# Optimization experiments

Hardware: AMD Instinct MI355X
Metric: run time of the kernel (lower is better)

## Reference

```python
import jax, jax.numpy as jnp
import numpy as np

T, B, D, H, HH, OUT = 512, 128, 256, 1024, 256, 128
EPS = 1e-3

def _ln(x, gamma, beta):
    # layer_norm over feature dim, eps=0.001, matching torch reciprocal(sqrt(var+eps))
    m = jnp.mean(x, -1, keepdims=True)
    xs = x - m
    v = jnp.mean(xs * xs, -1, keepdims=True)
    return gamma * xs * jax.lax.rsqrt(v + EPS) + beta

def _ln_all(h, base, units, gamma, beta):
    # normalize each of `base` gate blocks independently over `units`
    b = h.shape[0]
    hr = h.reshape(b, base, units)
    m = jnp.mean(hr, -1, keepdims=True)
    xs = hr - m
    v = jnp.mean(xs * xs, -1, keepdims=True)
    hn = (xs * jax.lax.rsqrt(v + EPS)).reshape(b, base * units)
    return gamma * hn + beta

def setup_inputs() -> dict:
    key = jax.random.key(0)
    ks = jax.random.split(key, 12)
    return {
        "x": jax.random.normal(ks[0], (T, B, D), jnp.float32),
        "Wx": jax.random.normal(ks[1], (4 * H, D), jnp.float32) * (1.0 / np.sqrt(D)),
        "Wh": jax.random.normal(ks[2], (4 * H, H), jnp.float32) * (1.0 / np.sqrt(H)),
        "bias": jax.random.normal(ks[3], (4 * H,), jnp.float32) * 0.1,
        "lna_gamma": jnp.ones((4 * H,), jnp.float32),
        "lna_beta": jnp.zeros((4 * H,), jnp.float32),
        "ln_gamma": jnp.ones((H,), jnp.float32),
        "ln_beta": jnp.zeros((H,), jnp.float32),
        "zb": jax.random.normal(ks[4], (4, HH, HH), jnp.float32) * 0.01,   # ib/jb/fb/ob _zb
        "zbeta": jax.random.normal(ks[5], (4, HH, H), jnp.float32) * 0.01, # ib/jb/fb/ob _beta
        "zw_w": jax.random.normal(ks[6], (8, HH, HH), jnp.float32) * 0.01, # ix,jx,fx,ox,ih,jh,fh,oh _zw_w
        "zw_b": jnp.ones((8, HH), jnp.float32),
        "alpha": jnp.full((8, HH, H), 0.1 / HH, jnp.float32) + jax.random.normal(ks[7], (8, HH, H), jnp.float32) * 1e-4,
        "hyp_Wx": jax.random.normal(ks[8], (4 * HH, D + H), jnp.float32) * (1.0 / np.sqrt(D + H)),
        "hyp_bx": jnp.zeros((4 * HH,), jnp.float32),
        "hyp_Wh": jax.random.normal(ks[9], (4 * HH, HH), jnp.float32) * (1.0 / np.sqrt(HH)),
        "hyp_bh": jnp.zeros((4 * HH,), jnp.float32),
        "hyp_lna_gamma": jnp.ones((4 * HH,), jnp.float32),
        "hyp_lna_beta": jnp.zeros((4 * HH,), jnp.float32),
        "hyp_ln_gamma": jnp.ones((HH,), jnp.float32),
        "hyp_ln_beta": jnp.zeros((HH,), jnp.float32),
        "fc_W": jax.random.normal(ks[10], (OUT, H), jnp.float32) * (1.0 / np.sqrt(H)),
        "fc_b": jnp.zeros((OUT,), jnp.float32),
    }

def reference(x, Wx, Wh, bias, lna_gamma, lna_beta, ln_gamma, ln_beta, zb, zbeta,
              zw_w, zw_b, alpha, hyp_Wx, hyp_bx, hyp_Wh, hyp_bh,
              hyp_lna_gamma, hyp_lna_beta, hyp_ln_gamma, hyp_ln_beta, fc_W, fc_b):
    b4 = bias.reshape(4, H)

    def step(carry, xt):
        h, c, hh, ch = carry  # main (B,H), hyper (B,HH)
        # ---- hypernetwork LSTM cell (layer-norm LSTM) ----
        g = jnp.concatenate([xt, h], 1) @ hyp_Wx.T + hyp_bx + hh @ hyp_Wh.T + hyp_bh
        g = _ln_all(g, 4, HH, hyp_lna_gamma, hyp_lna_beta)
        hi, hf, hg, ho = jnp.split(g, 4, 1)  # ingate, forgetgate, cellgate, outgate
        ch_n = jax.nn.sigmoid(hf) * ch + jax.nn.sigmoid(hi) * jnp.tanh(hg)
        hyp = jax.nn.sigmoid(ho) * jnp.tanh(_ln(ch_n, hyp_ln_gamma, hyp_ln_beta))
        # ---- hyper-modulation: per-gate scale vectors and bias adjustments ----
        z = jnp.einsum('bq,kqp->kbp', hyp, zw_w) + zw_b[:, None, :]   # (8,B,HH)
        sc = jnp.einsum('kbp,kph->kbh', z, alpha)                     # (8,B,H)
        bz = jnp.einsum('bq,kqp->kbp', hyp, zb)                       # (4,B,HH)
        badj = jnp.einsum('kbp,kph->kbh', bz, zbeta)                  # (4,B,H)
        # ---- main LSTM gates (order i, j, f, o) ----
        xg = (xt @ Wx.T).reshape(B, 4, H).transpose(1, 0, 2)          # (4,B,H)
        hg2 = (h @ Wh.T).reshape(B, 4, H).transpose(1, 0, 2)          # (4,B,H)
        gates = sc[:4] * xg + sc[4:] * hg2 + b4[:, None, :] + badj    # (4,B,H)
        gates = _ln_all(gates.transpose(1, 0, 2).reshape(B, 4 * H), 4, H, lna_gamma, lna_beta)
        i, j, f, o = jnp.split(gates, 4, 1)
        c_n = jax.nn.sigmoid(f) * c + jax.nn.sigmoid(i) * jnp.tanh(j)
        h_n = jax.nn.sigmoid(o) * jnp.tanh(_ln(c_n, ln_gamma, ln_beta))
        return (h_n, c_n, hyp, ch_n), None

    init = (jnp.zeros((B, H), x.dtype), jnp.zeros((B, H), x.dtype),
            jnp.zeros((B, HH), x.dtype), jnp.zeros((B, HH), x.dtype))
    (h_f, _, _, _), _ = jax.lax.scan(step, init, x)
    return h_f @ fc_W.T + fc_b  # (B, OUT)
```

## Files before the change

### kernel.cpp

```cpp
#include <hip/hip_runtime.h>
#include <hip/hip_cooperative_groups.h>
#include <math.h>

namespace cg = cooperative_groups;

#define T_STEPS 512
#define BATCH   128
#define DIN     256
#define HMAIN   1024
#define HHYP    256
#define OUTN    128
#define EPS     1e-3f

#define KSPLIT_NONE (1<<30)

typedef __attribute__((ext_vector_type(4))) float f32x4;
typedef __attribute__((ext_vector_type(8))) short s16x8;

__device__ __forceinline__ float sigm(float x){ return 1.f/(1.f + expf(-x)); }

__device__ __forceinline__ unsigned short f2bf(float f){
    union { float f; unsigned u; } x; x.f = f;
    unsigned r = x.u + 0x7FFFu + ((x.u >> 16) & 1u);
    return (unsigned short)(r >> 16);
}

#define BM 32
#define BN 64
#define KT 32
__device__ void gemm_dev(const float* __restrict__ A1, int lda1, int ksplit,
                         const float* __restrict__ A2, int lda2,
                         const float* __restrict__ Bp, int ldb, int b_nk,
                         const float* __restrict__ bias,
                         float* __restrict__ C, int ldc,
                         int K, int k0, int mtile, int ntile)
{
    __shared__ __align__(16) float As[KT][BM+4];
    __shared__ __align__(16) float Bs[KT][BN+4];
    const int tid = threadIdx.x;
    const int mt = tid >> 4, nt = tid & 15;
    const int m0g = mtile*BM, n0g = ntile*BN;
    float acc[4][4];
    #pragma unroll
    for (int i=0;i<4;++i) { acc[i][0]=0;acc[i][1]=0;acc[i][2]=0;acc[i][3]=0; }
    for (int kt = 0; kt < K; kt += KT) {
        __syncthreads();
        #pragma unroll
        for (int i=0;i<8;++i){
            int e = tid + i*128;
            int m = e >> 5, k = e & 31;
            int gk = k0 + kt + k, gm = m0g + m;
            float v = (gk < ksplit) ? A1[(size_t)gm*lda1 + gk]
                                    : A2[(size_t)gm*lda2 + (gk - ksplit)];
            As[k][m] = v;
        }
        if (b_nk) {
            #pragma unroll
            for (int i=0;i<16;++i){
                int e = tid + i*128;
                int n = e >> 5, k = e & 31;
                Bs[k][n] = Bp[(size_t)(n0g + n)*ldb + (k0 + kt + k)];
            }
        } else {
            #pragma unroll
            for (int i=0;i<16;++i){
                int e = tid + i*128;
                int k = e >> 6, n = e & 63;
                Bs[k][n] = Bp[(size_t)(k0 + kt + k)*ldb + (n0g + n)];
            }
        }
        __syncthreads();
        #pragma unroll
        for (int k=0;k<KT;++k){
            float4 av = *(const float4*)(&As[k][4*mt]);
            float4 bv = *(const float4*)(&Bs[k][4*nt]);
            acc[0][0]+=av.x*bv.x; acc[0][1]+=av.x*bv.y; acc[0][2]+=av.x*bv.z; acc[0][3]+=av.x*bv.w;
            acc[1][0]+=av.y*bv.x; acc[1][1]+=av.y*bv.y; acc[1][2]+=av.y*bv.z; acc[1][3]+=av.y*bv.w;
            acc[2][0]+=av.z*bv.x; acc[2][1]+=av.z*bv.y; acc[2][2]+=av.z*bv.z; acc[2][3]+=av.z*bv.w;
            acc[3][0]+=av.w*bv.x; acc[3][1]+=av.w*bv.y; acc[3][2]+=av.w*bv.z; acc[3][3]+=av.w*bv.w;
        }
    }
    #pragma unroll
    for (int i=0;i<4;++i){
        int gm = m0g + 4*mt + i;
        #pragma unroll
        for (int j=0;j<4;++j){
            int gn = n0g + 4*nt + j;
            float v = acc[i][j];
            if (bias) v += bias[gn];
            C[(size_t)gm*ldc + gn] = v;
        }
    }
}

#define ASTR 40
__device__ void gemm_mfma(const float* __restrict__ A1, int lda1, int ksplit,
                          const float* __restrict__ A2, int lda2,
                          const unsigned short* __restrict__ B, int ldb,
                          const float* __restrict__ bias,
                          float* __restrict__ C, int ldc,
                          int K, int k0, int mtile, int ntile)
{
    __shared__ __align__(16) unsigned short As[32*ASTR];
    __shared__ __align__(16) unsigned short Bs[128*ASTR];
    const int tid = threadIdx.x;
    const int lane = tid & 63, w = tid >> 6;
    const int wm = (w >> 1) * 16, wn = (w & 1) * 64;
    const int fr = lane & 15, koff = (lane >> 4) * 8;
    const int m0g = mtile*32, n0g = ntile*128;

    f32x4 acc[4];
    #pragma unroll
    for (int j=0;j<4;++j) acc[j] = (f32x4){0.f,0.f,0.f,0.f};

    const int arow = tid >> 3, akc = (tid & 7) * 4;
    for (int kt = 0; kt < K; kt += 32) {
        __syncthreads();
        {
            int gk = k0 + kt + akc;
            int gm = m0g + arow;
            const float* src = (gk < ksplit) ? (A1 + (size_t)gm*lda1 + gk)
                                             : (A2 + (size_t)gm*lda2 + (gk - ksplit));
            float4 v = *(const float4*)src;
            unsigned short* d = &As[arow*ASTR + akc];
            d[0] = f2bf(v.x); d[1] = f2bf(v.y); d[2] = f2bf(v.z); d[3] = f2bf(v.w);
        }
        #pragma unroll
        for (int i=0;i<4;++i){
            int e = tid + i*256;
            int n = e >> 3, kc = (e & 7) * 4;
            ushort4 bv = *(const ushort4*)(B + (size_t)(n0g + n)*ldb + (k0 + kt + kc));
            unsigned short* d = &Bs[n*ASTR + kc];
            d[0] = bv.x; d[1] = bv.y; d[2] = bv.z; d[3] = bv.w;
        }
        __syncthreads();
        s16x8 af = *(const s16x8*)&As[(wm + fr)*ASTR + koff];
        #pragma unroll
        for (int j=0;j<4;++j){
            s16x8 bf = *(const s16x8*)&Bs[(wn + j*16 + fr)*ASTR + koff];
            acc[j] = __builtin_amdgcn_mfma_f32_16x16x32_bf16(af, bf, acc[j], 0, 0, 0);
        }
    }
    #pragma unroll
    for (int j=0;j<4;++j){
        int gn = n0g + wn + j*16 + fr;
        float bb = bias ? bias[gn] : 0.f;
        #pragma unroll
        for (int r=0;r<4;++r){
            int gm = m0g + wm + (lane >> 4)*4 + r;
            C[(size_t)gm*ldc + gn] = acc[j][r] + bb;
        }
    }
}

__global__ __launch_bounds__(256) void k_prep_convert(
    const float* __restrict__ hyp_Wx, const float* __restrict__ hyp_Wh,
    const float* __restrict__ hyp_bx, const float* __restrict__ hyp_bh,
    const float* __restrict__ Wx, const float* __restrict__ Wh,
    unsigned short* __restrict__ wcat1bf, unsigned short* __restrict__ wxbf,
    unsigned short* __restrict__ whbf, float* __restrict__ bias1,
    float* __restrict__ act1, float* __restrict__ c, float* __restrict__ ch)
{
    size_t i = (size_t)blockIdx.x*256 + threadIdx.x;
    if (i < 1572864u) {
        int n = (int)(i / 1536), k = (int)(i % 1536);
        float v = (k < 1280) ? hyp_Wx[(size_t)n*1280 + k] : hyp_Wh[(size_t)n*256 + (k-1280)];
        wcat1bf[i] = f2bf(v); return;
    }
    i -= 1572864u;
    if (i < 1048576u) { wxbf[i] = f2bf(Wx[i]); return; }
    i -= 1048576u;
    if (i < 4194304u) { whbf[i] = f2bf(Wh[i]); return; }
    i -= 4194304u;
    if (i < 1024u) { bias1[i] = hyp_bx[i] + hyp_bh[i]; return; }
    i -= 1024u;
    if (i < 163840u) { act1[i] = 0.f; return; }
    i -= 163840u;
    if (i < 131072u) { c[i] = 0.f; return; }
    i -= 131072u;
    if (i < 32768u) { ch[i] = 0.f; return; }
}

__global__ __launch_bounds__(128) void k_prep_wcomb(
    const float* __restrict__ zw_w, const float* __restrict__ zb,
    const float* __restrict__ alpha, const float* __restrict__ zbeta,
    float* __restrict__ wcombf32)
{
    int kk = blockIdx.z;
    const float* A = (kk < 8) ? (zw_w + (size_t)kk*65536) : (zb + (size_t)(kk-8)*65536);
    const float* Bm = (kk < 8) ? (alpha + (size_t)kk*262144) : (zbeta + (size_t)(kk-8)*262144);
    gemm_dev(A, 256, KSPLIT_NONE, A, 256, Bm, 1024, 0, nullptr,
             wcombf32 + (size_t)kk*262144, 1024, 256, 0, blockIdx.x, blockIdx.y);
}

__global__ __launch_bounds__(256) void k_prep_cvtcomb(
    const float* __restrict__ wcombf32, unsigned short* __restrict__ wcombbf)
{
    size_t i = (size_t)blockIdx.x*256 + threadIdx.x;
    if (i >= 3145728u) return;
    int kk = (int)(i / 262144u);
    int r  = (int)(i % 262144u);
    int n = r / 256, k = r % 256;
    wcombbf[i] = f2bf(wcombf32[(size_t)kk*262144 + (size_t)k*1024 + n]);
}

__global__ __launch_bounds__(256) void k_prep_bcomb(
    const float* __restrict__ zw_b, const float* __restrict__ alpha,
    float* __restrict__ bcomb)
{
    int k = blockIdx.x;
    int n = blockIdx.y*256 + threadIdx.x;
    float s = 0.f;
    for (int p=0;p<256;++p)
        s += zw_b[k*256+p] * alpha[(size_t)k*262144 + (size_t)p*1024 + n];
    bcomb[(size_t)k*1024 + n] = s;
}

__device__ __forceinline__ void breduce2(float& a, float& b, volatile float* buf, int tid){
    #pragma unroll
    for (int off = 32; off > 0; off >>= 1) { a += __shfl_xor(a, off); b += __shfl_xor(b, off); }
    __syncthreads();
    if ((tid & 63) == 0) { buf[(tid>>6)*2] = a; buf[(tid>>6)*2+1] = b; }
    __syncthreads();
    a = buf[0] + buf[2] + buf[4] + buf[6];
    b = buf[1] + buf[3] + buf[5] + buf[7];
}

__device__ __forceinline__ void hyper_cell_body(
    const float* __restrict__ lna_g, const float* __restrict__ lna_b,
    const float* __restrict__ ln_g, const float* __restrict__ ln_b,
    const float* __restrict__ gpart, const float* __restrict__ bias1,
    float* __restrict__ ch, float* __restrict__ act1, int b, int tid)
{
    __shared__ float buf[8];
    float v[4];
    #pragma unroll
    for (int g=0; g<4; ++g){
        int idx = b*1024 + g*256 + tid;
        v[g] = gpart[idx] + gpart[131072 + idx] + gpart[262144 + idx] + gpart[393216 + idx]
             + bias1[g*256 + tid];
    }
    #pragma unroll
    for (int g=0; g<4; ++g){
        float s = v[g], ss = v[g]*v[g];
        breduce2(s, ss, buf, tid);
        float m = s * (1.f/256.f);
        float var = ss * (1.f/256.f) - m*m;
        v[g] = (v[g]-m)*rsqrtf(var + EPS)*lna_g[g*256+tid] + lna_b[g*256+tid];
    }
    float chp = ch[b*256 + tid];
    float cn = sigm(v[1])*chp + sigm(v[0])*tanhf(v[2]);
    float s = cn, ss = cn*cn;
    breduce2(s, ss, buf, tid);
    float m = s*(1.f/256.f);
    float var = ss*(1.f/256.f) - m*m;
    float hn = sigm(v[3]) * tanhf((cn-m)*rsqrtf(var + EPS)*ln_g[tid] + ln_b[tid]);
    ch[b*256 + tid] = cn;
    act1[b*1280 + 1024 + tid] = hn;
}

__device__ __forceinline__ void main_cell_body(
    const float* __restrict__ bias4,
    const float* __restrict__ lna_g, const float* __restrict__ lna_b,
    const float* __restrict__ ln_g, const float* __restrict__ ln_b,
    const float* __restrict__ xghg, const float* __restrict__ scb,
    float* __restrict__ c, float* __restrict__ act1, int b, int tid)
{
    __shared__ float buf[8];
    float gn[4][4];
    #pragma unroll
    for (int k=0;k<4;++k){
        float pre[4]; float s=0.f, ss=0.f;
        #pragma unroll
        for (int j=0;j<4;++j){
            int h = j*256 + tid;
            int n = k*1024 + h;
            int bh = b*1024 + h;
            float xgv = xghg[b*4096 + n];
            float hgv = xghg[524288 + b*4096 + n];
            float p = scb[k*131072 + bh]*xgv + scb[(4+k)*131072 + bh]*hgv
                    + bias4[n] + scb[(8+k)*131072 + bh];
            pre[j] = p; s += p; ss += p*p;
        }
        breduce2(s, ss, buf, tid);
        float m = s*(1.f/1024.f);
        float var = ss*(1.f/1024.f) - m*m;
        float rs = rsqrtf(var + EPS);
        #pragma unroll
        for (int j=0;j<4;++j){
            int h=j*256+tid, n=k*1024+h;
            gn[k][j] = (pre[j]-m)*rs*lna_g[n] + lna_b[n];
        }
    }
    float cnv[4]; float s=0.f, ss=0.f;
    #pragma unroll
    for (int j=0;j<4;++j){
        int h=j*256+tid;
        float cv = c[b*1024+h];
        float x = sigm(gn[2][j])*cv + sigm(gn[0][j])*tanhf(gn[1][j]);
        cnv[j]=x; s+=x; ss+=x*x;
    }
    breduce2(s, ss, buf, tid);
    float m=s*(1.f/1024.f);
    float var=ss*(1.f/1024.f)-m*m;
    float rs=rsqrtf(var + EPS);
    #pragma unroll
    for (int j=0;j<4;++j){
        int h=j*256+tid;
        float hv = sigm(gn[3][j])*tanhf((cnv[j]-m)*rs*ln_g[h] + ln_b[h]);
        c[b*1024+h] = cnv[j];
        act1[b*1280 + h] = hv;
    }
}

__global__ __launch_bounds__(256) void k_step1(
    const float* __restrict__ xt, const float* __restrict__ act1,
    const unsigned short* __restrict__ wcat1bf,
    const unsigned short* __restrict__ wxbf, const unsigned short* __restrict__ whbf,
    float* __restrict__ gpart, float* __restrict__ xghg)
{
    int bid = blockIdx.x;
    if (bid < 128) {
        int sp = bid >> 5, r = bid & 31;
        gemm_mfma(xt, 256, 256, act1, 1280, wcat1bf, 1536, nullptr,
                  gpart + (size_t)sp*131072, 1024, 384, sp*384, r >> 3, r & 7);
    } else if (bid < 256) {
        int r = bid - 128;
        gemm_mfma(xt, 256, KSPLIT_NONE, xt, 256, wxbf, 256, nullptr,
                  xghg, 4096, 256, 0, r >> 5, r & 31);
    } else {
        int r = bid - 256;
        gemm_mfma(act1, 1280, KSPLIT_NONE, act1, 1280, whbf, 1024, nullptr,
                  xghg + 524288, 4096, 1024, 0, r >> 5, r & 31);
    }
}

__global__ __launch_bounds__(256) void k_step2(
    const float* __restrict__ act1, const unsigned short* __restrict__ wcombbf,
    const float* __restrict__ bcomb, float* __restrict__ scb)
{
    int bid = blockIdx.x;
    int kk = bid >> 5, r = bid & 31;
    const float* bias = (kk < 8) ? (bcomb + (size_t)kk*1024) : nullptr;
    gemm_mfma(act1 + 1024, 1280, KSPLIT_NONE, act1 + 1024, 1280,
              wcombbf + (size_t)kk*262144, 256, bias,
              scb + (size_t)kk*131072, 1024, 256, 0, r >> 3, r & 7);
}

__global__ __launch_bounds__(256) void k_hyper_cell(
    const float* __restrict__ lna_g, const float* __restrict__ lna_b,
    const float* __restrict__ ln_g, const float* __restrict__ ln_b,
    const float* __restrict__ gpart, const float* __restrict__ bias1,
    float* __restrict__ ch, float* __restrict__ act1)
{
    hyper_cell_body(lna_g, lna_b, ln_g, ln_b, gpart, bias1, ch, act1,
                    blockIdx.x, threadIdx.x);
}

__global__ __launch_bounds__(256) void k_main_cell(
    const float* __restrict__ bias4,
    const float* __restrict__ lna_g, const float* __restrict__ lna_b,
    const float* __restrict__ ln_g, const float* __restrict__ ln_b,
    const float* __restrict__ xghg, const float* __restrict__ scb,
    float* __restrict__ c, float* __restrict__ act1)
{
    main_cell_body(bias4, lna_g, lna_b, ln_g, ln_b, xghg, scb, c, act1,
                   blockIdx.x, threadIdx.x);
}

__global__ __launch_bounds__(256, 2) void k_persistent(
    const float* __restrict__ x,
    const unsigned short* __restrict__ wcat1bf,
    const unsigned short* __restrict__ wxbf,
    const unsigned short* __restrict__ whbf,
    const unsigned short* __restrict__ wcombbf,
    const float* __restrict__ bcomb,
    const float* __restrict__ bias1,
    const float* __restrict__ bias4,
    const float* __restrict__ lna_g, const float* __restrict__ lna_b,
    const float* __restrict__ ln_g, const float* __restrict__ ln_b,
    const float* __restrict__ hlna_g, const float* __restrict__ hlna_b,
    const float* __restrict__ hln_g, const float* __restrict__ hln_b,
    float* __restrict__ gpart, float* __restrict__ scb,
    float* __restrict__ xghg, float* __restrict__ act1,
    float* __restrict__ c, float* __restrict__ ch)
{
    cg::grid_group grid = cg::this_grid();
    const int bid = blockIdx.x;
    const int tid = threadIdx.x;

    for (int t = 0; t < T_STEPS; ++t) {
        const float* xt = x + (size_t)t*BATCH*DIN;

        if (bid < 128) {
            int sp = bid >> 5, r = bid & 31;
            gemm_mfma(xt, 256, 256, act1, 1280, wcat1bf, 1536, nullptr,
                      gpart + (size_t)sp*131072, 1024, 384, sp*384, r >> 3, r & 7);
        } else if (bid < 256) {
            int r = bid - 128;
            gemm_mfma(xt, 256, KSPLIT_NONE, xt, 256, wxbf, 256, nullptr,
                      xghg, 4096, 256, 0, r >> 5, r & 31);
        } else {
            int r = bid - 256;
            gemm_mfma(act1, 1280, KSPLIT_NONE, act1, 1280, whbf, 1024, nullptr,
                      xghg + 524288, 4096, 1024, 0, r >> 5, r & 31);
        }
        grid.sync();

        if (bid < 128)
            hyper_cell_body(hlna_g, hlna_b, hln_g, hln_b, gpart, bias1, ch, act1, bid, tid);
        grid.sync();

        {
            int kk = bid >> 5, r = bid & 31;
            const float* bias = (kk < 8) ? (bcomb + (size_t)kk*1024) : nullptr;
            gemm_mfma(act1 + 1024, 1280, KSPLIT_NONE, act1 + 1024, 1280,
                      wcombbf + (size_t)kk*262144, 256, bias,
                      scb + (size_t)kk*131072, 1024, 256, 0, r >> 3, r & 7);
        }
        grid.sync();

        if (bid < 128)
            main_cell_body(bias4, lna_g, lna_b, ln_g, ln_b, xghg, scb, c, act1, bid, tid);
        grid.sync();
    }
}

__global__ __launch_bounds__(128) void k_fc(
    const float* __restrict__ fcW, const float* __restrict__ fcb,
    const float* __restrict__ act1, float* __restrict__ out)
{
    int b = blockIdx.x, o = threadIdx.x;
    const float* h = act1 + (size_t)b*1280;
    float s = fcb[o];
    for (int k=0;k<1024;++k) s += h[k]*fcW[(size_t)o*1024 + k];
    out[b*OUTN + o] = s;
}

extern "C" void kernel_launch(void* const* d_in, const int* in_sizes, int n_in,
                              void* d_out, int out_size, void* d_ws, size_t ws_size,
                              hipStream_t stream)
{
    const float* x        = (const float*)d_in[0];
    const float* Wx       = (const float*)d_in[1];
    const float* Wh       = (const float*)d_in[2];
    const float* bias     = (const float*)d_in[3];
    const float* lna_g    = (const float*)d_in[4];
    const float* lna_b    = (const float*)d_in[5];
    const float* ln_g     = (const float*)d_in[6];
    const float* ln_b     = (const float*)d_in[7];
    const float* zb       = (const float*)d_in[8];
    const float* zbeta    = (const float*)d_in[9];
    const float* zw_w     = (const float*)d_in[10];
    const float* zw_b     = (const float*)d_in[11];
    const float* alpha    = (const float*)d_in[12];
    const float* hyp_Wx   = (const float*)d_in[13];
    const float* hyp_bx   = (const float*)d_in[14];
    const float* hyp_Wh   = (const float*)d_in[15];
    const float* hyp_bh   = (const float*)d_in[16];
    const float* hlna_g   = (const float*)d_in[17];
    const float* hlna_b   = (const float*)d_in[18];
    const float* hln_g    = (const float*)d_in[19];
    const float* hln_b    = (const float*)d_in[20];
    const float* fcW      = (const float*)d_in[21];
    const float* fcb      = (const float*)d_in[22];
    float* out = (float*)d_out;

    unsigned short* wcat1bf = (unsigned short*)d_ws;
    unsigned short* wxbf    = wcat1bf + 1572864;
    unsigned short* whbf    = wxbf + 1048576;
    unsigned short* wcombbf = whbf + 4194304;
    float* bcomb = (float*)(wcombbf + 3145728);
    float* bias1 = bcomb + 8192;
    float* act1  = bias1 + 1024;
    float* c     = act1 + 163840;
    float* ch    = c + 131072;
    float* stepbuf = ch + 32768;
    float* gpart = stepbuf;
    float* scb   = gpart + 524288;
    float* xghg  = scb + 1572864;
    float* wcombf32 = stepbuf;

    k_prep_convert<<<(7144448 + 255)/256, 256, 0, stream>>>(
        hyp_Wx, hyp_Wh, hyp_bx, hyp_bh, Wx, Wh,
        wcat1bf, wxbf, whbf, bias1, act1, c, ch);
    k_prep_wcomb<<<dim3(8,16,12), 128, 0, stream>>>(zw_w, zb, alpha, zbeta, wcombf32);
    k_prep_bcomb<<<dim3(8,4), 256, 0, stream>>>(zw_b, alpha, bcomb);
    k_prep_cvtcomb<<<(3145728 + 255)/256, 256, 0, stream>>>(wcombf32, wcombbf);

    static int use_coop = -1;
    if (use_coop < 0) {
        use_coop = 0;
        int dev = 0;
        if (hipGetDevice(&dev) == hipSuccess) {
            hipDeviceProp_t prop;
            if (hipGetDeviceProperties(&prop, dev) == hipSuccess &&
                prop.cooperativeLaunch) {
                int occ = 0;
                if (hipOccupancyMaxActiveBlocksPerMultiprocessor(
                        &occ, (const void*)k_persistent, 256, 0) == hipSuccess &&
                    occ * prop.multiProcessorCount >= 384) {
                    use_coop = 1;
                }
            }
        }
    }

    int coop_launched = 0;
    if (use_coop) {
        void* cargs[] = {
            (void*)&x, (void*)&wcat1bf, (void*)&wxbf, (void*)&whbf, (void*)&wcombbf,
            (void*)&bcomb, (void*)&bias1, (void*)&bias,
            (void*)&lna_g, (void*)&lna_b, (void*)&ln_g, (void*)&ln_b,
            (void*)&hlna_g, (void*)&hlna_b, (void*)&hln_g, (void*)&hln_b,
            (void*)&gpart, (void*)&scb, (void*)&xghg, (void*)&act1,
            (void*)&c, (void*)&ch
        };
        hipError_t e = hipLaunchCooperativeKernel((const void*)k_persistent,
                                                  dim3(384), dim3(256),
                                                  cargs, 0u, stream);
        if (e == hipSuccess) {
            coop_launched = 1;
        } else {
            (void)hipGetLastError();
            use_coop = 0;
        }
    }

    if (!coop_launched) {
        for (int t = 0; t < T_STEPS; ++t) {
            const float* xt = x + (size_t)t*BATCH*DIN;
            k_step1<<<384, 256, 0, stream>>>(xt, act1, wcat1bf, wxbf, whbf, gpart, xghg);
            k_hyper_cell<<<BATCH, 256, 0, stream>>>(hlna_g, hlna_b, hln_g, hln_b,
                                                    gpart, bias1, ch, act1);
            k_step2<<<384, 256, 0, stream>>>(act1, wcombbf, bcomb, scb);
            k_main_cell<<<BATCH, 256, 0, stream>>>(bias, lna_g, lna_b, ln_g, ln_b,
                                                   xghg, scb, c, act1);
        }
    }

    k_fc<<<BATCH, 128, 0, stream>>>(fcW, fcb, act1, out);
}
```

Baseline: 34.28 ms.

## Keep weight tiles resident in LDS across timesteps in persistent kernel

Rewrites the persistent cooperative kernel so each of 512 blocks loads its slice of the bf16 weight matrices into shared memory once, then reuses it for every timestep through a new full-K GEMM helper. Activations are stored in bf16 so GEMM operands need no per-step conversion. The stage schedule changes: the hyper GEMM uses 6-way K split, the main hidden GEMM uses 4-way K split with partials summed in the cell, and hyper-cell work overlaps with the main gate GEMMs. The goal is to remove repeated global weight traffic per step, at the cost of more grid syncs' worth of partial buffers, ~50KB LDS per block, and a requirement of 2 resident blocks per CU.

```diff
diff --git a/kernel.cpp b/kernel.cpp
--- a/kernel.cpp
+++ b/kernel.cpp
@@ -153,13 +153,80 @@
     }
 }
 
+#define WSTR 264
+template<int NF, bool AF32>
+__device__ __forceinline__ void gemm_ws(
+    const void* __restrict__ Aptr, int lda,
+    const unsigned short* wtile,
+    const float* __restrict__ bias,
+    float* __restrict__ Cout, int ldc,
+    int lane, int w)
+{
+    const int fr = lane & 15, kq = lane >> 4;
+    f32x4 acc[2][NF];
+    #pragma unroll
+    for (int mf=0; mf<2; ++mf)
+        #pragma unroll
+        for (int nf=0; nf<NF; ++nf) acc[mf][nf] = (f32x4){0.f,0.f,0.f,0.f};
+    const int r0 = w*32 + fr;
+    #pragma unroll
+    for (int kt=0; kt<256; kt+=32) {
+        const int k = kt + kq*8;
+        s16x8 a[2];
+        #pragma unroll
+        for (int mf=0; mf<2; ++mf) {
+            const int row = r0 + mf*16;
+            if (AF32) {
+                const float* s = (const float*)Aptr + (size_t)row*lda + k;
+                float4 v0 = *(const float4*)s;
+                float4 v1 = *(const float4*)(s+4);
+                union { s16x8 v; unsigned short u[8]; } tc;
+                tc.u[0]=f2bf(v0.x); tc.u[1]=f2bf(v0.y); tc.u[2]=f2bf(v0.z); tc.u[3]=f2bf(v0.w);
+                tc.u[4]=f2bf(v1.x); tc.u[5]=f2bf(v1.y); tc.u[6]=f2bf(v1.z); tc.u[7]=f2bf(v1.w);
+                a[mf] = tc.v;
+            } else {
+                a[mf] = *(const s16x8*)((const unsigned short*)Aptr + (size_t)row*lda + k);
+            }
+        }
+        #pragma unroll
+        for (int nf=0; nf<NF; ++nf) {
+            s16x8 b = *(const s16x8*)&wtile[(nf*16+fr)*WSTR + k];
+            acc[0][nf] = __builtin_amdgcn_mfma_f32_16x16x32_bf16(a[0], b, acc[0][nf], 0,0,0);
+            acc[1][nf] = __builtin_amdgcn_mfma_f32_16x16x32_bf16(a[1], b, acc[1][nf], 0,0,0);
+        }
+    }
+    #pragma unroll
+    for (int nf=0; nf<NF; ++nf) {
+        const int col = nf*16 + fr;
+        const float bb = bias ? bias[col] : 0.f;
+        #pragma unroll
+        for (int mf=0; mf<2; ++mf) {
+            const int row = w*32 + mf*16 + kq*4;
+            #pragma unroll
+            for (int r=0; r<4; ++r)
+                Cout[(size_t)(row+r)*ldc + col] = acc[mf][nf][r] + bb;
+        }
+    }
+}
+
+__device__ __forceinline__ void load_wtile(const unsigned short* __restrict__ src,
+                                           int ld, unsigned short* dst, int rows, int tid)
+{
+    const int chunks = rows * 32;
+    for (int cidx = tid; cidx < chunks; cidx += 256) {
+        const int r = cidx >> 5, k8 = (cidx & 31) << 3;
+        *(uint4*)&dst[r*WSTR + k8] = *(const uint4*)&src[(size_t)r*ld + k8];
+    }
+}
+
 __global__ __launch_bounds__(256) void k_prep_convert(
     const float* __restrict__ hyp_Wx, const float* __restrict__ hyp_Wh,
     const float* __restrict__ hyp_bx, const float* __restrict__ hyp_bh,
     const float* __restrict__ Wx, const float* __restrict__ Wh,
     unsigned short* __restrict__ wcat1bf, unsigned short* __restrict__ wxbf,
     unsigned short* __restrict__ whbf, float* __restrict__ bias1,
-    float* __restrict__ act1, float* __restrict__ c, float* __restrict__ ch)
+    float* __restrict__ act1f, float* __restrict__ c, float* __restrict__ ch,
+    unsigned int* __restrict__ act1bf_zero)
 {
     size_t i = (size_t)blockIdx.x*256 + threadIdx.x;
     if (i < 1572864u) {
@@ -174,12 +241,15 @@
     i -= 4194304u;
     if (i < 1024u) { bias1[i] = hyp_bx[i] + hyp_bh[i]; return; }
     i -= 1024u;
-    if (i < 163840u) { act1[i] = 0.f; return; }
+    if (i < 163840u) { act1f[i] = 0.f; return; }
     i -= 163840u;
     if (i < 131072u) { c[i] = 0.f; return; }
     i -= 131072u;
     if (i < 32768u) { ch[i] = 0.f; return; }
-}
+    i -= 32768u;
+    if (i < 81920u && act1bf_zero) { act1bf_zero[i] = 0u; return; }
+}
+#define PREP_TOTAL 7225568u
 
 __global__ __launch_bounds__(128) void k_prep_wcomb(
     const float* __restrict__ zw_w, const float* __restrict__ zb,
@@ -224,6 +294,98 @@
     __syncthreads();
     a = buf[0] + buf[2] + buf[4] + buf[6];
     b = buf[1] + buf[3] + buf[5] + buf[7];
+}
+
+__device__ __forceinline__ void hyper_cell6(
+    int b, int tid, volatile float* cbuf,
+    const float* __restrict__ gpart, const float* __restrict__ bias1,
+    const float* __restrict__ lna_g, const float* __restrict__ lna_b,
+    const float* __restrict__ ln_g, const float* __restrict__ ln_b,
+    float* __restrict__ ch, unsigned short* __restrict__ act1bf)
+{
+    float v[4];
+    #pragma unroll
+    for (int g=0; g<4; ++g){
+        size_t idx = (size_t)b*1024 + g*256 + tid;
+        v[g] = gpart[idx] + gpart[131072+idx] + gpart[262144+idx]
+             + gpart[393216+idx] + gpart[524288+idx] + gpart[655360+idx]
+             + bias1[g*256 + tid];
+    }
+    #pragma unroll
+    for (int g=0; g<4; ++g){
+        float s = v[g], ss = v[g]*v[g];
+        breduce2(s, ss, cbuf, tid);
+        float m = s * (1.f/256.f);
+        float var = ss * (1.f/256.f) - m*m;
+        v[g] = (v[g]-m)*rsqrtf(var + EPS)*lna_g[g*256+tid] + lna_b[g*256+tid];
+    }
+    float chp = ch[b*256 + tid];
+    float cn = sigm(v[1])*chp + sigm(v[0])*tanhf(v[2]);
+    float s = cn, ss = cn*cn;
+    breduce2(s, ss, cbuf, tid);
+    float m = s*(1.f/256.f);
+    float var = ss*(1.f/256.f) - m*m;
+    float hn = sigm(v[3]) * tanhf((cn-m)*rsqrtf(var + EPS)*ln_g[tid] + ln_b[tid]);
+    ch[b*256 + tid] = cn;
+    act1bf[(size_t)b*1280 + 1024 + tid] = f2bf(hn);
+}
+
+__device__ __forceinline__ void main_cell2(
+    int b, int tid, volatile float* cbuf,
+    const float* __restrict__ bias4,
+    const float* __restrict__ lna_g, const float* __restrict__ lna_b,
+    const float* __restrict__ ln_g, const float* __restrict__ ln_b,
+    const float* __restrict__ xgbuf, const float* __restrict__ hgpart,
+    const float* __restrict__ scb,
+    float* __restrict__ c, unsigned short* __restrict__ act1bf,
+    float* __restrict__ hfc)
+{
+    float gn[4][4];
+    #pragma unroll
+    for (int k=0;k<4;++k){
+        float pre[4]; float s=0.f, ss=0.f;
+        #pragma unroll
+        for (int j=0;j<4;++j){
+            int h = j*256 + tid;
+            int n = k*1024 + h;
+            size_t bh = (size_t)b*1024 + h;
+            size_t bn = (size_t)b*4096 + n;
+            float xgv = xgbuf[bn];
+            float hgv = hgpart[bn] + hgpart[524288+bn] + hgpart[1048576+bn] + hgpart[1572864+bn];
+            float p = scb[(size_t)k*131072 + bh]*xgv + scb[(size_t)(4+k)*131072 + bh]*hgv
+                    + bias4[n] + scb[(size_t)(8+k)*131072 + bh];
+            pre[j] = p; s += p; ss += p*p;
+        }
+        breduce2(s, ss, cbuf, tid);
+        float m = s*(1.f/1024.f);
+        float var = ss*(1.f/1024.f) - m*m;
+        float rs = rsqrtf(var + EPS);
+        #pragma unroll
+        for (int j=0;j<4;++j){
+            int h=j*256+tid, n=k*1024+h;
+            gn[k][j] = (pre[j]-m)*rs*lna_g[n] + lna_b[n];
+        }
+    }
+    float cnv[4]; float s=0.f, ss=0.f;
+    #pragma unroll
+    for (int j=0;j<4;++j){
+        int h=j*256+tid;
+        float cv = c[(size_t)b*1024+h];
+        float x = sigm(gn[2][j])*cv + sigm(gn[0][j])*tanhf(gn[1][j]);
+        cnv[j]=x; s+=x; ss+=x*x;
+    }
+    breduce2(s, ss, cbuf, tid);
+    float m=s*(1.f/1024.f);
+    float var=ss*(1.f/1024.f)-m*m;
+    float rs=rsqrtf(var + EPS);
+    #pragma unroll
+    for (int j=0;j<4;++j){
+        int h=j*256+tid;
+        float hv = sigm(gn[3][j])*tanhf((cnv[j]-m)*rs*ln_g[h] + ln_b[h]);
+        c[(size_t)b*1024+h] = cnv[j];
+        act1bf[(size_t)b*1280 + h] = f2bf(hv);
+        hfc[(size_t)b*1024 + h] = hv;
+    }
 }
 
 __device__ __forceinline__ void hyper_cell_body(
@@ -368,70 +530,95 @@
                    blockIdx.x, threadIdx.x);
 }
 
-__global__ __launch_bounds__(256, 2) void k_persistent(
+__global__ __launch_bounds__(256, 2) void k_persist2(
     const float* __restrict__ x,
     const unsigned short* __restrict__ wcat1bf,
     const unsigned short* __restrict__ wxbf,
     const unsigned short* __restrict__ whbf,
     const unsigned short* __restrict__ wcombbf,
-    const float* __restrict__ bcomb,
-    const float* __restrict__ bias1,
+    const float* __restrict__ bcomb, const float* __restrict__ bias1,
     const float* __restrict__ bias4,
     const float* __restrict__ lna_g, const float* __restrict__ lna_b,
     const float* __restrict__ ln_g, const float* __restrict__ ln_b,
     const float* __restrict__ hlna_g, const float* __restrict__ hlna_b,
     const float* __restrict__ hln_g, const float* __restrict__ hln_b,
-    float* __restrict__ gpart, float* __restrict__ scb,
-    float* __restrict__ xghg, float* __restrict__ act1,
+    float* __restrict__ gpart, float* __restrict__ hgpart,
+    float* __restrict__ xgbuf, float* __restrict__ scb,
+    unsigned short* __restrict__ act1bf, float* __restrict__ hfc,
     float* __restrict__ c, float* __restrict__ ch)
 {
     cg::grid_group grid = cg::this_grid();
-    const int bid = blockIdx.x;
-    const int tid = threadIdx.x;
+    const int bid = blockIdx.x, tid = threadIdx.x;
+    const int lane = tid & 63, w = tid >> 6;
+    __shared__ __align__(16) unsigned short wlds[25344];
+    __shared__ float cbuf[8];
+
+    if (bid < 96) {
+        load_wtile(wcat1bf + (size_t)((bid & 15)*64)*1536 + (bid >> 4)*256,
+                   1536, wlds, 64, tid);
+    } else if (bid < 352) {
+        int h_ = bid - 96;
+        load_wtile(whbf + (size_t)((h_ >> 2)*64)*1024 + (h_ & 3)*256,
+                   1024, wlds, 64, tid);
+    } else if (bid < 416) {
+        load_wtile(wxbf + (size_t)(bid - 352)*64*256, 256, wlds, 64, tid);
+    }
+    if (bid < 384) {
+        int kk = bid >> 5, mt = bid & 31;
+        load_wtile(wcombbf + (size_t)kk*262144 + (size_t)(mt*32)*256,
+                   256, wlds + 16896, 32, tid);
+    }
+    __syncthreads();
 
     for (int t = 0; t < T_STEPS; ++t) {
         const float* xt = x + (size_t)t*BATCH*DIN;
 
-        if (bid < 128) {
-            int sp = bid >> 5, r = bid & 31;
-            gemm_mfma(xt, 256, 256, act1, 1280, wcat1bf, 1536, nullptr,
-                      gpart + (size_t)sp*131072, 1024, 384, sp*384, r >> 3, r & 7);
-        } else if (bid < 256) {
-            int r = bid - 128;
-            gemm_mfma(xt, 256, KSPLIT_NONE, xt, 256, wxbf, 256, nullptr,
-                      xghg, 4096, 256, 0, r >> 5, r & 31);
+        if (bid < 96) {
+            int nt = bid & 15, sp = bid >> 4;
+            float* outp = gpart + (size_t)sp*131072 + nt*64;
+            if (sp == 0)
+                gemm_ws<4,true >(xt, 256, wlds, nullptr, outp, 1024, lane, w);
+            else
+                gemm_ws<4,false>(act1bf + (sp-1)*256, 1280, wlds, nullptr, outp, 1024, lane, w);
+        }
+        grid.sync();
+
+        if (bid >= 96 && bid < 352) {
+            int h_ = bid - 96, nt = h_ >> 2, sp = h_ & 3;
+            gemm_ws<4,false>(act1bf + sp*256, 1280, wlds, nullptr,
+                             hgpart + (size_t)sp*524288 + nt*64, 4096, lane, w);
+        } else if (bid >= 352 && bid < 416) {
+            gemm_ws<4,true >(xt, 256, wlds, nullptr,
+                             xgbuf + (bid - 352)*64, 4096, lane, w);
         } else {
-            int r = bid - 256;
-            gemm_mfma(act1, 1280, KSPLIT_NONE, act1, 1280, whbf, 1024, nullptr,
-                      xghg + 524288, 4096, 1024, 0, r >> 5, r & 31);
+            int row = (bid >= 416) ? (bid - 416) : (bid < 32 ? 96 + bid : -1);
+            if (row >= 0)
+                hyper_cell6(row, tid, cbuf, gpart, bias1,
+                            hlna_g, hlna_b, hln_g, hln_b, ch, act1bf);
         }
         grid.sync();
 
+        if (bid < 384) {
+            int kk = bid >> 5, mt = bid & 31;
+            const float* bp = (kk < 8) ? (bcomb + (size_t)kk*1024 + mt*32) : nullptr;
+            gemm_ws<2,false>(act1bf + 1024, 1280, wlds + 16896, bp,
+                             scb + (size_t)kk*131072 + mt*32, 1024, lane, w);
+        }
+        grid.sync();
+
         if (bid < 128)
-            hyper_cell_body(hlna_g, hlna_b, hln_g, hln_b, gpart, bias1, ch, act1, bid, tid);
+            main_cell2(bid, tid, cbuf, bias4, lna_g, lna_b, ln_g, ln_b,
+                       xgbuf, hgpart, scb, c, act1bf, hfc);
         grid.sync();
-
-        {
-            int kk = bid >> 5, r = bid & 31;
-            const float* bias = (kk < 8) ? (bcomb + (size_t)kk*1024) : nullptr;
-            gemm_mfma(act1 + 1024, 1280, KSPLIT_NONE, act1 + 1024, 1280,
-                      wcombbf + (size_t)kk*262144, 256, bias,
-                      scb + (size_t)kk*131072, 1024, 256, 0, r >> 3, r & 7);
-        }
-        grid.sync();
-
-        if (bid < 128)
-            main_cell_body(bias4, lna_g, lna_b, ln_g, ln_b, xghg, scb, c, act1, bid, tid);
-        grid.sync();
-    }
-}
-
-__global__ __launch_bounds__(128) void k_fc(
+    }
+}
+
+__global__ __launch_bounds__(128) void k_fc2(
     const float* __restrict__ fcW, const float* __restrict__ fcb,
-    const float* __restrict__ act1, float* __restrict__ out)
+    const float* __restrict__ hsrc, int ldh, float* __restrict__ out)
 {
     int b = blockIdx.x, o = threadIdx.x;
-    const float* h = act1 + (size_t)b*1280;
+    const float* h = hsrc + (size_t)b*ldh;
     float s = fcb[o];
     for (int k=0;k<1024;++k) s += h[k]*fcW[(size_t)o*1024 + k];
     out[b*OUTN + o] = s;
@@ -470,20 +657,23 @@
     unsigned short* wxbf    = wcat1bf + 1572864;
     unsigned short* whbf    = wxbf + 1048576;
     unsigned short* wcombbf = whbf + 4194304;
-    float* bcomb = (float*)(wcombbf + 3145728);
+    unsigned short* act1bf  = wcombbf + 3145728;
+    float* fbase = (float*)(act1bf + 163840);
+    float* bcomb = fbase;
     float* bias1 = bcomb + 8192;
-    float* act1  = bias1 + 1024;
-    float* c     = act1 + 163840;
+    float* hfc   = bias1 + 1024;
+    float* c     = hfc + 131072;
     float* ch    = c + 131072;
-    float* stepbuf = ch + 32768;
-    float* gpart = stepbuf;
-    float* scb   = gpart + 524288;
-    float* xghg  = scb + 1572864;
-    float* wcombf32 = stepbuf;
-
-    k_prep_convert<<<(7144448 + 255)/256, 256, 0, stream>>>(
+    float* act1o = ch + 32768;
+    float* gpart = act1o + 163840;
+    float* hgpart= gpart + 786432;
+    float* xgbuf = hgpart + 2097152;
+    float* scb   = xgbuf + 524288;
+    float* wcombf32 = gpart;
+
+    k_prep_convert<<<(PREP_TOTAL + 255)/256, 256, 0, stream>>>(
         hyp_Wx, hyp_Wh, hyp_bx, hyp_bh, Wx, Wh,
-        wcat1bf, wxbf, whbf, bias1, act1, c, ch);
+        wcat1bf, wxbf, whbf, bias1, act1o, c, ch, (unsigned int*)act1bf);
     k_prep_wcomb<<<dim3(8,16,12), 128, 0, stream>>>(zw_w, zb, alpha, zbeta, wcombf32);
     k_prep_bcomb<<<dim3(8,4), 256, 0, stream>>>(zw_b, alpha, bcomb);
     k_prep_cvtcomb<<<(3145728 + 255)/256, 256, 0, stream>>>(wcombf32, wcombbf);
@@ -498,8 +688,8 @@
                 prop.cooperativeLaunch) {
                 int occ = 0;
                 if (hipOccupancyMaxActiveBlocksPerMultiprocessor(
-                        &occ, (const void*)k_persistent, 256, 0) == hipSuccess &&
-                    occ * prop.multiProcessorCount >= 384) {
+                        &occ, (const void*)k_persist2, 256, 0) == hipSuccess &&
+                    occ >= 2 && occ * prop.multiProcessorCount >= 512) {
                     use_coop = 1;
                 }
             }
@@ -513,11 +703,11 @@
             (void*)&bcomb, (void*)&bias1, (void*)&bias,
             (void*)&lna_g, (void*)&lna_b, (void*)&ln_g, (void*)&ln_b,
             (void*)&hlna_g, (void*)&hlna_b, (void*)&hln_g, (void*)&hln_b,
-            (void*)&gpart, (void*)&scb, (void*)&xghg, (void*)&act1,
-            (void*)&c, (void*)&ch
+            (void*)&gpart, (void*)&hgpart, (void*)&xgbuf, (void*)&scb,
+            (void*)&act1bf, (void*)&hfc, (void*)&c, (void*)&ch
         };
-        hipError_t e = hipLaunchCooperativeKernel((const void*)k_persistent,
-                                                  dim3(384), dim3(256),
+        hipError_t e = hipLaunchCooperativeKernel((const void*)k_persist2,
+                                                  dim3(512), dim3(256),
                                                   cargs, 0u, stream);
         if (e == hipSuccess) {
             coop_launched = 1;
@@ -528,16 +718,19 @@
     }
 
     if (!coop_launched) {
+        float* xghg = hgpart;
         for (int t = 0; t < T_STEPS; ++t) {
             const float* xt = x + (size_t)t*BATCH*DIN;
-            k_step1<<<384, 256, 0, stream>>>(xt, act1, wcat1bf, wxbf, whbf, gpart, xghg);
+            k_step1<<<384, 256, 0, stream>>>(xt, act1o, wcat1bf, wxbf, whbf, gpart, xghg);
             k_hyper_cell<<<BATCH, 256, 0, stream>>>(hlna_g, hlna_b, hln_g, hln_b,
-                                                    gpart, bias1, ch, act1);
-            k_step2<<<384, 256, 0, stream>>>(act1, wcombbf, bcomb, scb);
+                                                    gpart, bias1, ch, act1o);
+            k_step2<<<384, 256, 0, stream>>>(act1o, wcombbf, bcomb, scb);
             k_main_cell<<<BATCH, 256, 0, stream>>>(bias, lna_g, lna_b, ln_g, ln_b,
-                                                   xghg, scb, c, act1);
-        }
-    }
-
-    k_fc<<<BATCH, 128, 0, stream>>>(fcW, fcb, act1, out);
-}
+                                                   xghg, scb, c, act1o);
+        }
+        k_fc2<<<BATCH, 128, 0, stream>>>(fcW, fcb, act1o, 1280, out);
+        return;
+    }
+
+    k_fc2<<<BATCH, 128, 0, stream>>>(fcW, fcb, hfc, 1024, out);
+}
```

New measurement: 34.20 ms. About the same (-0.2%).
